# Kernel tuning notes

Measured on AMD Instinct MI355X. Metric: run time of the kernel, lower is better.

## Reference

```python
import jax, jax.numpy as jnp
import numpy as np

D = 1024
H = 8
K = 6
TEMP = 0.1
LN_EPS = 1e-5


def _ln(x, g, b):
    m = jnp.mean(x, axis=-1, keepdims=True)
    v = jnp.mean((x - m) ** 2, axis=-1, keepdims=True)
    return (x - m) / jnp.sqrt(v + LN_EPS) * g + b


def setup_inputs() -> dict:
    key = jax.random.key(0)
    ks = jax.random.split(key, 8)
    B, T = 8, 4096
    s = 0.02
    inp = {
        'video_features': jax.random.normal(ks[0], (B, T, D), jnp.float32),
        'query_embedding': jax.random.normal(ks[1], (B, D), jnp.float32),
        'mu_w1': jax.random.normal(ks[2], (D, D), jnp.float32) * s,
        'mu_b1': jnp.zeros((D,), jnp.float32),
        'mu_g': jnp.ones((D,), jnp.float32),
        'mu_be': jnp.zeros((D,), jnp.float32),
        'mu_w2': jax.random.normal(ks[3], (D, D), jnp.float32) * s,
        'mu_b2': jnp.zeros((D,), jnp.float32),
        'sg_w1': jax.random.normal(ks[4], (D, D), jnp.float32) * s,
        'sg_b1': jnp.zeros((D,), jnp.float32),
        'sg_g': jnp.ones((D,), jnp.float32),
        'sg_be': jnp.zeros((D,), jnp.float32),
        'sg_w2': jax.random.normal(ks[5], (D, D), jnp.float32) * s,
        'sg_b2': jnp.zeros((D,), jnp.float32),
        'in_w': jax.random.normal(ks[6], (3 * D, D), jnp.float32) * s,
        'in_b': jnp.zeros((3 * D,), jnp.float32),
        'out_w': jax.random.normal(ks[7], (D, D), jnp.float32) * s,
        'out_b': jnp.zeros((D,), jnp.float32),
    }
    return inp


def reference(video_features, query_embedding, mu_w1, mu_b1, mu_g, mu_be, mu_w2, mu_b2,
              sg_w1, sg_b1, sg_g, sg_be, sg_w2, sg_b2, in_w, in_b, out_w, out_b):
    B, T, _ = video_features.shape
    dh = D // H

    # mu / sigma estimators (Linear -> LN -> ReLU -> Linear [-> Softplus])
    mu_q = jax.nn.relu(_ln(query_embedding @ mu_w1.T + mu_b1, mu_g, mu_be)) @ mu_w2.T + mu_b2  # [B,D]
    sigma_q = jax.nn.softplus(
        jax.nn.relu(_ln(query_embedding @ sg_w1.T + sg_b1, sg_g, sg_be)) @ sg_w2.T + sg_b2) + 1e-6

    # Mahalanobis (diagonal) distances [B,T]
    centered = video_features - mu_q[:, None, :]
    dist = jnp.sum(centered ** 2 / sigma_q[:, None, :], axis=-1)

    # distance weights around the (torch lower) median
    med = jnp.sort(dist, axis=1)[:, (T - 1) // 2][:, None]
    dist_w = jnp.exp(-jnp.abs(dist - med) / TEMP)  # [B,T]

    # single-query multihead attention (torch MHA, averaged attn weights)
    wq, wk, wv = in_w[:D], in_w[D:2 * D], in_w[2 * D:]
    bq, bk, bv = in_b[:D], in_b[D:2 * D], in_b[2 * D:]
    q = (mu_q @ wq.T + bq).reshape(B, H, dh)                  # [B,H,dh]
    k = (video_features @ wk.T + bk).reshape(B, T, H, dh)     # [B,T,H,dh]
    scores = jnp.einsum('bhd,bthd->bht', q, k) / jnp.sqrt(jnp.asarray(dh, q.dtype))
    attn = jax.nn.softmax(scores, axis=-1)                    # [B,H,T]
    attn_w = jnp.mean(attn, axis=1)                           # [B,T] head-averaged

    combined = dist_w * attn_w  # [B,T]

    # greedy diverse top-k (farthest-point style), vectorized over batch
    ar = jnp.arange(T)
    idx0 = jnp.argmax(combined, axis=1)                       # [B]
    sel_mask = ar[None, :] == idx0[:, None]
    min_d = jnp.abs(ar[None, :] - idx0[:, None]).astype(combined.dtype)
    picks = [idx0]
    for _ in range(K - 1):
        score = jnp.where(sel_mask, -jnp.inf, min_d * combined)
        nxt = jnp.argmax(score, axis=1)
        picks.append(nxt)
        sel_mask = sel_mask | (ar[None, :] == nxt[:, None])
        min_d = jnp.minimum(min_d, jnp.abs(ar[None, :] - nxt[:, None]).astype(combined.dtype))
    indices = jnp.stack(picks, axis=1)  # [B,K]

    rep = jnp.take_along_axis(video_features, indices[:, :, None], axis=1)  # [B,K,D]

    # NTLBG loss
    rep_dist = jnp.take_along_axis(dist, indices, axis=1)  # [B,K]
    target = jnp.sort(rep_dist, axis=1)[:, (K - 1) // 2][:, None]
    ellipsoid = jnp.mean((rep_dist - target) ** 2)
    centered_rep = rep - mu_q[:, None, :]
    consistency = jnp.mean(jnp.sum(centered_rep ** 2 / sigma_q[:, None, :], axis=-1))
    sim = jnp.einsum('bkd,bjd->bkj', rep, rep)
    tri = jnp.triu(jnp.ones((K, K), rep.dtype), k=1)
    diversity = jnp.mean((sim * tri) ** 2)
    loss = ellipsoid + 0.1 * consistency + 0.05 * diversity

    return rep, indices, combined, dist, mu_q, sigma_q, loss
```

## Files before the change

### kernel.cpp

```cpp
#include <hip/hip_runtime.h>
#include <math.h>

#define BD   8
#define TT   4096
#define DD   1024
#define HH   8
#define KK   6
#define OFF_REP   0
#define OFF_IDX   49152
#define OFF_COMB  49200
#define OFF_DIST  81968
#define OFF_MU    114736
#define OFF_SG    122928
#define OFF_LOSS  131120
#define WS_X1     0
#define WS_H      16384
#define WS_Q      32768
#define WS_P      40960
#define WS_C      106496
#define WS_ISIG   106560
#define WS_SCORES 114752

#define INV_SQRT_DH 0.08838834764831845f

__device__ __forceinline__ float softplus_f(float x) {
  return fmaxf(x, 0.0f) + log1pf(expf(-fabsf(x)));
}

__device__ __forceinline__ void gemv_rows_core(const float* __restrict__ in,
                                               const float* __restrict__ W,
                                               int row, float (*s_in)[DD], float acc[8]) {
  int tid = threadIdx.x;
  const float4* in4 = (const float4*)in;
  float4* s4 = (float4*)&s_in[0][0];
  for (int i = tid; i < 2048; i += 256) s4[i] = in4[i];
  __syncthreads();
  int lane = tid & 63;
  const float4* wr4 = (const float4*)(W + (size_t)row * DD);
#pragma unroll
  for (int b = 0; b < 8; ++b) acc[b] = 0.0f;
#pragma unroll
  for (int i = 0; i < 4; ++i) {
    int d4 = i * 64 + lane;
    float4 w4 = wr4[d4];
#pragma unroll
    for (int b = 0; b < 8; ++b) {
      float4 q4 = ((const float4*)&s_in[b][0])[d4];
      acc[b] += w4.x * q4.x + w4.y * q4.y + w4.z * q4.z + w4.w * q4.w;
    }
  }
#pragma unroll
  for (int off = 32; off; off >>= 1)
#pragma unroll
    for (int b = 0; b < 8; ++b) acc[b] += __shfl_xor(acc[b], off, 64);
}

__global__ __launch_bounds__(256) void k_gemv_pre(const float* __restrict__ qe,
    const float* __restrict__ W0, const float* __restrict__ W1,
    const float* __restrict__ b0, const float* __restrict__ b1, float* __restrict__ x1) {
  __shared__ float s_in[8][DD];
  int path = blockIdx.x >> 8;
  int row = (blockIdx.x & 255) * 4 + (threadIdx.x >> 6);
  const float* W = path ? W1 : W0;
  const float* bb = path ? b1 : b0;
  float acc[8];
  gemv_rows_core(qe, W, row, s_in, acc);
  if ((threadIdx.x & 63) == 0) {
    float bv = bb[row];
#pragma unroll
    for (int b = 0; b < 8; ++b) x1[path * 8192 + b * DD + row] = acc[b] + bv;
  }
}

__global__ __launch_bounds__(256) void k_ln(const float* __restrict__ x1,
    const float* __restrict__ g0, const float* __restrict__ be0,
    const float* __restrict__ g1, const float* __restrict__ be1, float* __restrict__ h) {
  int path = blockIdx.x >> 3, b = blockIdx.x & 7;
  const float* x = x1 + path * 8192 + b * DD;
  const float* g = path ? g1 : g0;
  const float* be = path ? be1 : be0;
  __shared__ float sx[DD];
  __shared__ float red[256];
  int tid = threadIdx.x;
  float ps = 0.0f;
  for (int i = tid; i < DD; i += 256) { float v = x[i]; sx[i] = v; ps += v; }
  red[tid] = ps; __syncthreads();
  for (int off = 128; off; off >>= 1) { if (tid < off) red[tid] += red[tid + off]; __syncthreads(); }
  float mean = red[0] * (1.0f / 1024.0f);
  __syncthreads();
  float pv = 0.0f;
  for (int i = tid; i < DD; i += 256) { float d = sx[i] - mean; pv += d * d; }
  red[tid] = pv; __syncthreads();
  for (int off = 128; off; off >>= 1) { if (tid < off) red[tid] += red[tid + off]; __syncthreads(); }
  float var = red[0] * (1.0f / 1024.0f);
  float inv = 1.0f / sqrtf(var + 1e-5f);
  for (int i = tid; i < DD; i += 256) {
    float v = (sx[i] - mean) * inv * g[i] + be[i];
    h[path * 8192 + b * DD + i] = v > 0.0f ? v : 0.0f;
  }
}

__global__ __launch_bounds__(256) void k_gemv_mid(const float* __restrict__ h,
    const float* __restrict__ W0, const float* __restrict__ W1,
    const float* __restrict__ b0, const float* __restrict__ b1,
    float* __restrict__ mu_out, float* __restrict__ sg_out, float* __restrict__ isig) {
  __shared__ float s_in[8][DD];
  int path = blockIdx.x >> 8;
  int row = (blockIdx.x & 255) * 4 + (threadIdx.x >> 6);
  const float* W = path ? W1 : W0;
  const float* bb = path ? b1 : b0;
  float acc[8];
  gemv_rows_core(h + path * 8192, W, row, s_in, acc);
  if ((threadIdx.x & 63) == 0) {
    float bv = bb[row];
#pragma unroll
    for (int b = 0; b < 8; ++b) {
      float v = acc[b] + bv;
      if (path == 0) {
        mu_out[b * DD + row] = v;
      } else {
        float sp = softplus_f(v) + 1e-6f;
        sg_out[b * DD + row] = sp;
        isig[b * DD + row] = 1.0f / sp;
      }
    }
  }
}

__global__ __launch_bounds__(256) void k_gemv_q(const float* __restrict__ mu_q,
    const float* __restrict__ in_w, const float* __restrict__ in_b, float* __restrict__ q) {
  __shared__ float s_in[8][DD];
  int row = blockIdx.x * 4 + (threadIdx.x >> 6);
  float acc[8];
  gemv_rows_core(mu_q, in_w, row, s_in, acc);
  if ((threadIdx.x & 63) == 0) {
    float bv = in_b[row];
#pragma unroll
    for (int b = 0; b < 8; ++b) q[b * DD + row] = acc[b] + bv;
  }
}

__global__ __launch_bounds__(256) void k_p(const float* __restrict__ q,
    const float* __restrict__ in_w, const float* __restrict__ in_b,
    float* __restrict__ p, float* __restrict__ c) {
  int hh = blockIdx.x >> 2;
  int j0 = (blockIdx.x & 3) * 256;
  __shared__ float qh[8][128];
  for (int i = threadIdx.x; i < 1024; i += 256) {
    int b = i >> 7, r = i & 127;
    qh[b][r] = q[b * DD + hh * 128 + r];
  }
  __syncthreads();
  const float* wbase = in_w + (size_t)(DD + hh * 128) * DD + j0 + threadIdx.x;
  float acc[8];
#pragma unroll
  for (int b = 0; b < 8; ++b) acc[b] = 0.0f;
  for (int r = 0; r < 128; ++r) {
    float w = wbase[(size_t)r * DD];
#pragma unroll
    for (int b = 0; b < 8; ++b) acc[b] += qh[b][r] * w;
  }
#pragma unroll
  for (int b = 0; b < 8; ++b) p[(b * HH + hh) * DD + j0 + threadIdx.x] = acc[b] * INV_SQRT_DH;
  if ((blockIdx.x & 3) == 0 && threadIdx.x < 8) {
    int b = threadIdx.x;
    float cc = 0.0f;
    for (int r = 0; r < 128; ++r) cc += qh[b][r] * in_b[DD + hh * 128 + r];
    c[b * HH + hh] = cc * INV_SQRT_DH;
  }
}

__global__ __launch_bounds__(256, 4) void k_main(const float* __restrict__ video,
    const float* __restrict__ mu_q, const float* __restrict__ isig,
    const float* __restrict__ p, const float* __restrict__ c,
    float* __restrict__ dist_out, float* __restrict__ scores, float* __restrict__ loss_out) {
  __shared__ float s_mu[DD];
  __shared__ float s_is[DD];
  __shared__ float s_p[HH][DD];
  int b = blockIdx.x >> 8;
  int chunk = blockIdx.x & 255;
  int tid = threadIdx.x;
  int wave = tid >> 6, lane = tid & 63;
  if (blockIdx.x == 0 && tid == 0) loss_out[0] = 0.0f;
  float4* s_mu4 = (float4*)s_mu;
  float4* s_is4 = (float4*)s_is;
  float4* s_p4 = (float4*)&s_p[0][0];
  s_mu4[tid] = ((const float4*)(mu_q + b * DD))[tid];
  s_is4[tid] = ((const float4*)(isig + b * DD))[tid];
  const float4* pg4 = (const float4*)(p + b * HH * DD);
  for (int i = tid; i < 2048; i += 256) s_p4[i] = pg4[i];
  __syncthreads();

  int t0 = chunk * 16 + wave * 4;
  const float4* v4 = (const float4*)(video + ((size_t)(b * TT + t0)) * DD);
  double dacc[4] = {0.0, 0.0, 0.0, 0.0};
  float sacc[4][8];
#pragma unroll
  for (int t = 0; t < 4; ++t)
#pragma unroll
    for (int hh = 0; hh < 8; ++hh) sacc[t][hh] = 0.0f;

#pragma unroll 2
  for (int i = 0; i < 4; ++i) {
    int d4 = i * 64 + lane;
    float4 vv0 = v4[0 * 256 + d4];
    float4 vv1 = v4[1 * 256 + d4];
    float4 vv2 = v4[2 * 256 + d4];
    float4 vv3 = v4[3 * 256 + d4];
    {
      float4 mu4 = s_mu4[d4];
      float4 is4 = s_is4[d4];
      float dx, dy, dz, dw, e;
      dx = vv0.x - mu4.x; dy = vv0.y - mu4.y; dz = vv0.z - mu4.z; dw = vv0.w - mu4.w;
      e = dx * dx * is4.x + dy * dy * is4.y + dz * dz * is4.z + dw * dw * is4.w;
      dacc[0] += (double)e;
      dx = vv1.x - mu4.x; dy = vv1.y - mu4.y; dz = vv1.z - mu4.z; dw = vv1.w - mu4.w;
      e = dx * dx * is4.x + dy * dy * is4.y + dz * dz * is4.z + dw * dw * is4.w;
      dacc[1] += (double)e;
      dx = vv2.x - mu4.x; dy = vv2.y - mu4.y; dz = vv2.z - mu4.z; dw = vv2.w - mu4.w;
      e = dx * dx * is4.x + dy * dy * is4.y + dz * dz * is4.z + dw * dw * is4.w;
      dacc[2] += (double)e;
      dx = vv3.x - mu4.x; dy = vv3.y - mu4.y; dz = vv3.z - mu4.z; dw = vv3.w - mu4.w;
      e = dx * dx * is4.x + dy * dy * is4.y + dz * dz * is4.z + dw * dw * is4.w;
      dacc[3] += (double)e;
    }
#pragma unroll
    for (int hh = 0; hh < 8; ++hh) {
      float4 pp = ((const float4*)&s_p[hh][0])[d4];
      sacc[0][hh] += pp.x * vv0.x + pp.y * vv0.y + pp.z * vv0.z + pp.w * vv0.w;
      sacc[1][hh] += pp.x * vv1.x + pp.y * vv1.y + pp.z * vv1.z + pp.w * vv1.w;
      sacc[2][hh] += pp.x * vv2.x + pp.y * vv2.y + pp.z * vv2.z + pp.w * vv2.w;
      sacc[3][hh] += pp.x * vv3.x + pp.y * vv3.y + pp.z * vv3.z + pp.w * vv3.w;
    }
  }
#pragma unroll
  for (int off = 32; off; off >>= 1) {
#pragma unroll
    for (int t = 0; t < 4; ++t) {
      dacc[t] += __shfl_xor(dacc[t], off, 64);
#pragma unroll
      for (int hh = 0; hh < 8; ++hh) sacc[t][hh] += __shfl_xor(sacc[t][hh], off, 64);
    }
  }
  if (lane < 4) {
    int t = lane;
    int tt = t0 + t;
    dist_out[b * TT + tt] = (float)dacc[t];
#pragma unroll
    for (int hh = 0; hh < 8; ++hh)
      scores[(size_t)(b * HH + hh) * TT + tt] = sacc[t][hh] + c[b * HH + hh];
  }
}

__global__ __launch_bounds__(256) void k_epilogue(const float* __restrict__ scores,
    const float* __restrict__ dist, const float* __restrict__ video,
    float* __restrict__ comb_out, float* __restrict__ idx_out,
    float* __restrict__ rep, float* __restrict__ loss_out) {
  int b = blockIdx.x;
  int tid = threadIdx.x;
  int wave = tid >> 6, lane = tid & 63;
  __shared__ float s_aw[TT];
  __shared__ float s_comb[TT];
  __shared__ float s_mind[TT];
  __shared__ float s_dist[TT];
  __shared__ float s_hm[HH], s_hs[HH];
  __shared__ unsigned hist[256];
  __shared__ unsigned wsum[4];
  __shared__ unsigned s_sel;
  __shared__ int s_kk;
  __shared__ float wv[4];
  __shared__ int wi[4];
  __shared__ int s_pick;
  __shared__ float wdiv[4];

  {
    int h = tid >> 5, lt = tid & 31;
    const float* srow = scores + ((size_t)(b * HH + h)) * TT;
    float m = -INFINITY;
    for (int i = lt; i < TT; i += 32) m = fmaxf(m, srow[i]);
#pragma unroll
    for (int off = 16; off; off >>= 1) m = fmaxf(m, __shfl_xor(m, off, 64));
    float s = 0.0f;
    for (int i = lt; i < TT; i += 32) s += expf(srow[i] - m);
#pragma unroll
    for (int off = 16; off; off >>= 1) s += __shfl_xor(s, off, 64);
    if (lt == 0) { s_hm[h] = m; s_hs[h] = 1.0f / s; }
  }
  __syncthreads();
  for (int i = tid; i < TT; i += 256) {
    float aw = 0.0f;
#pragma unroll
    for (int h = 0; h < HH; ++h)
      aw += expf(scores[((size_t)(b * HH + h)) * TT + i] - s_hm[h]) * s_hs[h];
    s_aw[i] = aw * 0.125f;
    s_dist[i] = dist[b * TT + i];
  }
  __syncthreads();

  unsigned prefix = 0;
  int kk = (TT - 1) / 2;
  for (int pass = 0; pass < 4; ++pass) {
    int shift = 24 - 8 * pass;
    hist[tid] = 0;
    __syncthreads();
    for (int i = tid; i < TT; i += 256) {
      unsigned key = __float_as_uint(s_dist[i]);
      bool ok = (pass == 0) || ((key >> (shift + 8)) == prefix);
      if (ok) atomicAdd(&hist[(key >> shift) & 255], 1u);
    }
    __syncthreads();
    unsigned h = hist[tid];
    unsigned inc = h;
#pragma unroll
    for (int off = 1; off < 64; off <<= 1) {
      unsigned v = __shfl_up(inc, off, 64);
      if (lane >= off) inc += v;
    }
    if (lane == 63) wsum[wave] = inc;
    __syncthreads();
    unsigned base = 0;
    for (int w = 0; w < wave; ++w) base += wsum[w];
    unsigned excl = base + inc - h;
    if ((int)excl <= kk && kk < (int)(excl + h)) { s_sel = (prefix << 8) | (unsigned)tid; s_kk = kk - (int)excl; }
    __syncthreads();
    prefix = s_sel;
    kk = s_kk;
    __syncthreads();
  }
  float med = __uint_as_float(prefix);

  for (int i = tid; i < TT; i += 256) {
    float cv = expf(-fabsf(s_dist[i] - med) / 0.1f) * s_aw[i];
    s_comb[i] = cv;
    comb_out[b * TT + i] = cv;
  }
  __syncthreads();

  int picks[KK];
  for (int k = 0; k < KK; ++k) {
    float best = -INFINITY; int bi = 1 << 30;
    for (int i = tid; i < TT; i += 256) {
      float cv = s_comb[i];
      float sc = (k == 0) ? cv : ((cv < 0.0f) ? -INFINITY : s_mind[i] * cv);
      if (sc > best) { best = sc; bi = i; }
    }
#pragma unroll
    for (int off = 32; off; off >>= 1) {
      float ov = __shfl_xor(best, off, 64);
      int oi = __shfl_xor(bi, off, 64);
      if (ov > best || (ov == best && oi < bi)) { best = ov; bi = oi; }
    }
    if (lane == 0) { wv[wave] = best; wi[wave] = bi; }
    __syncthreads();
    if (tid == 0) {
      float bb2 = wv[0]; int ii = wi[0];
#pragma unroll
      for (int w = 1; w < 4; ++w)
        if (wv[w] > bb2 || (wv[w] == bb2 && wi[w] < ii)) { bb2 = wv[w]; ii = wi[w]; }
      s_pick = ii;
      s_comb[ii] = -1.0f;
    }
    __syncthreads();
    int pick = s_pick;
    picks[k] = pick;
    for (int i = tid; i < TT; i += 256) {
      float dnew = fabsf((float)(i - pick));
      s_mind[i] = (k == 0) ? dnew : fminf(s_mind[i], dnew);
    }
  }
  if (tid < KK) idx_out[b * KK + tid] = (float)picks[tid];

  __shared__ float repb[KK * DD];
  float4* repb4 = (float4*)repb;
  float4* rep4 = (float4*)(rep + (size_t)b * KK * DD);
  for (int e = tid; e < KK * (DD / 4); e += 256) {
    int k = e >> 8, d4 = e & 255;
    const float4* vrow = (const float4*)(video + ((size_t)(b * TT + picks[0])) * DD);
    vrow = (const float4*)(video + ((size_t)(b * TT + picks[e >> 8])) * DD);
    float4 v = vrow[d4];
    rep4[(size_t)k * (DD / 4) + d4] = v;
    repb4[k * (DD / 4) + d4] = v;
  }
  __syncthreads();
  const int pk[15] = {0,0,0,0,0,1,1,1,1,2,2,2,3,3,4};
  const int pj[15] = {1,2,3,4,5,2,3,4,5,3,4,5,4,5,5};
  float divacc = 0.0f;
  for (int pid = wave; pid < 15; pid += 4) {
    int a = pk[pid], j = pj[pid];
    float part = 0.0f;
    for (int d = lane; d < DD; d += 64) part += repb[a * DD + d] * repb[j * DD + d];
#pragma unroll
    for (int off = 32; off; off >>= 1) part += __shfl_xor(part, off, 64);
    if (lane == 0) divacc += part * part;
  }
  if (lane == 0) wdiv[wave] = divacc;
  __syncthreads();
  if (tid == 0) {
    float div = wdiv[0] + wdiv[1] + wdiv[2] + wdiv[3];
    float rd[KK], srt[KK];
#pragma unroll
    for (int k = 0; k < KK; ++k) { rd[k] = s_dist[picks[k]]; srt[k] = rd[k]; }
    for (int a = 1; a < KK; ++a) {
      float key = srt[a]; int b2 = a - 1;
      while (b2 >= 0 && srt[b2] > key) { srt[b2 + 1] = srt[b2]; --b2; }
      srt[b2 + 1] = key;
    }
    float target = srt[(KK - 1) / 2];
    float ell = 0.0f, cons = 0.0f;
#pragma unroll
    for (int k = 0; k < KK; ++k) { float d = rd[k] - target; ell += d * d; cons += rd[k]; }
    float partial = ell * (1.0f / 48.0f) + 0.1f * cons * (1.0f / 48.0f) + 0.05f * div * (1.0f / 288.0f);
    atomicAdd(loss_out, partial);
  }
}

extern "C" void kernel_launch(void* const* d_in, const int* in_sizes, int n_in,
                              void* d_out, int out_size, void* d_ws, size_t ws_size,
                              hipStream_t stream) {
  const float* video = (const float*)d_in[0];
  const float* qe    = (const float*)d_in[1];
  const float* mu_w1 = (const float*)d_in[2];
  const float* mu_b1 = (const float*)d_in[3];
  const float* mu_g  = (const float*)d_in[4];
  const float* mu_be = (const float*)d_in[5];
  const float* mu_w2 = (const float*)d_in[6];
  const float* mu_b2 = (const float*)d_in[7];
  const float* sg_w1 = (const float*)d_in[8];
  const float* sg_b1 = (const float*)d_in[9];
  const float* sg_g  = (const float*)d_in[10];
  const float* sg_be = (const float*)d_in[11];
  const float* sg_w2 = (const float*)d_in[12];
  const float* sg_b2 = (const float*)d_in[13];
  const float* in_w  = (const float*)d_in[14];
  const float* in_b  = (const float*)d_in[15];
  float* out = (float*)d_out;
  float* ws  = (float*)d_ws;

  k_gemv_pre<<<512, 256, 0, stream>>>(qe, mu_w1, sg_w1, mu_b1, sg_b1, ws + WS_X1);
  k_ln<<<16, 256, 0, stream>>>(ws + WS_X1, mu_g, mu_be, sg_g, sg_be, ws + WS_H);
  k_gemv_mid<<<512, 256, 0, stream>>>(ws + WS_H, mu_w2, sg_w2, mu_b2, sg_b2,
                                      out + OFF_MU, out + OFF_SG, ws + WS_ISIG);
  k_gemv_q<<<256, 256, 0, stream>>>(out + OFF_MU, in_w, in_b, ws + WS_Q);
  k_p<<<32, 256, 0, stream>>>(ws + WS_Q, in_w, in_b, ws + WS_P, ws + WS_C);
  k_main<<<2048, 256, 0, stream>>>(video, out + OFF_MU, ws + WS_ISIG, ws + WS_P, ws + WS_C,
                                   out + OFF_DIST, ws + WS_SCORES, out + OFF_LOSS);
  k_epilogue<<<8, 256, 0, stream>>>(ws + WS_SCORES, out + OFF_DIST, video,
                                    out + OFF_COMB, out + OFF_IDX, out + OFF_REP, out + OFF_LOSS);
}
```

Baseline: 380.7 us.

## Widen epilogue to 1024 threads with register-resident per-thread elements

The per-batch epilogue kernel grows from 256 to 1024 threads. Each thread now keeps four timesteps (distance, attention weight, combined score, min-distance) in registers, read with float4 loads, in place of shared-memory arrays. The softmax reductions, radix-select histogram and greedy farthest-point argmax loops are rewritten for the wider block, and the diversity dot products get one wave per pair. The aim is to cut the serial latency of this 8-block, latency-bound tail, at the cost of more per-block synchronisation across 16 waves.

```diff
diff --git a/kernel.cpp b/kernel.cpp
--- a/kernel.cpp
+++ b/kernel.cpp
@@ -252,76 +252,111 @@
   }
 }
 
-__global__ __launch_bounds__(256) void k_epilogue(const float* __restrict__ scores,
+__global__ __launch_bounds__(1024) void k_epilogue(const float* __restrict__ scores,
     const float* __restrict__ dist, const float* __restrict__ video,
     float* __restrict__ comb_out, float* __restrict__ idx_out,
     float* __restrict__ rep, float* __restrict__ loss_out) {
   int b = blockIdx.x;
   int tid = threadIdx.x;
   int wave = tid >> 6, lane = tid & 63;
-  __shared__ float s_aw[TT];
-  __shared__ float s_comb[TT];
-  __shared__ float s_mind[TT];
   __shared__ float s_dist[TT];
   __shared__ float s_hm[HH], s_hs[HH];
+  __shared__ float s_w16[16], s_w16b[16];
   __shared__ unsigned hist[256];
   __shared__ unsigned wsum[4];
   __shared__ unsigned s_sel;
   __shared__ int s_kk;
-  __shared__ float wv[4];
-  __shared__ int wi[4];
+  __shared__ float wv[16];
+  __shared__ int wi[16];
   __shared__ int s_pick;
-  __shared__ float wdiv[4];
+  __shared__ float wdiv[16];
+  __shared__ float repb[KK * DD];
 
   {
-    int h = tid >> 5, lt = tid & 31;
-    const float* srow = scores + ((size_t)(b * HH + h)) * TT;
+    int h = tid >> 7, lt = tid & 127;
+    const float4* srow4 = (const float4*)(scores + ((size_t)(b * HH + h)) * TT);
     float m = -INFINITY;
-    for (int i = lt; i < TT; i += 32) m = fmaxf(m, srow[i]);
-#pragma unroll
-    for (int off = 16; off; off >>= 1) m = fmaxf(m, __shfl_xor(m, off, 64));
+#pragma unroll
+    for (int i = 0; i < 8; ++i) {
+      float4 v = srow4[lt + i * 128];
+      m = fmaxf(m, fmaxf(fmaxf(v.x, v.y), fmaxf(v.z, v.w)));
+    }
+#pragma unroll
+    for (int off = 32; off; off >>= 1) m = fmaxf(m, __shfl_xor(m, off, 64));
+    if (lane == 0) s_w16[wave] = m;
+    __syncthreads();
+    float mh = fmaxf(s_w16[h * 2], s_w16[h * 2 + 1]);
     float s = 0.0f;
-    for (int i = lt; i < TT; i += 32) s += expf(srow[i] - m);
-#pragma unroll
-    for (int off = 16; off; off >>= 1) s += __shfl_xor(s, off, 64);
-    if (lt == 0) { s_hm[h] = m; s_hs[h] = 1.0f / s; }
-  }
-  __syncthreads();
-  for (int i = tid; i < TT; i += 256) {
-    float aw = 0.0f;
-#pragma unroll
-    for (int h = 0; h < HH; ++h)
-      aw += expf(scores[((size_t)(b * HH + h)) * TT + i] - s_hm[h]) * s_hs[h];
-    s_aw[i] = aw * 0.125f;
-    s_dist[i] = dist[b * TT + i];
-  }
+#pragma unroll
+    for (int i = 0; i < 8; ++i) {
+      float4 v = srow4[lt + i * 128];
+      s += expf(v.x - mh) + expf(v.y - mh) + expf(v.z - mh) + expf(v.w - mh);
+    }
+#pragma unroll
+    for (int off = 32; off; off >>= 1) s += __shfl_xor(s, off, 64);
+    if (lane == 0) s_w16b[wave] = s;
+    __syncthreads();
+    if (lt == 0) { s_hm[h] = mh; s_hs[h] = 1.0f / (s_w16b[h * 2] + s_w16b[h * 2 + 1]); }
+    __syncthreads();
+  }
+
+  float4 d4 = ((const float4*)(dist + b * TT))[tid];
+  ((float4*)s_dist)[tid] = d4;
+  float4 aw = make_float4(0.f, 0.f, 0.f, 0.f);
+#pragma unroll
+  for (int h = 0; h < HH; ++h) {
+    float4 sc = ((const float4*)(scores + ((size_t)(b * HH + h)) * TT))[tid];
+    float mh = s_hm[h], is = s_hs[h];
+    aw.x += expf(sc.x - mh) * is;
+    aw.y += expf(sc.y - mh) * is;
+    aw.z += expf(sc.z - mh) * is;
+    aw.w += expf(sc.w - mh) * is;
+  }
+  aw.x *= 0.125f; aw.y *= 0.125f; aw.z *= 0.125f; aw.w *= 0.125f;
+  uint4 keys;
+  keys.x = __float_as_uint(d4.x);
+  keys.y = __float_as_uint(d4.y);
+  keys.z = __float_as_uint(d4.z);
+  keys.w = __float_as_uint(d4.w);
   __syncthreads();
 
   unsigned prefix = 0;
   int kk = (TT - 1) / 2;
   for (int pass = 0; pass < 4; ++pass) {
     int shift = 24 - 8 * pass;
-    hist[tid] = 0;
-    __syncthreads();
-    for (int i = tid; i < TT; i += 256) {
-      unsigned key = __float_as_uint(s_dist[i]);
-      bool ok = (pass == 0) || ((key >> (shift + 8)) == prefix);
-      if (ok) atomicAdd(&hist[(key >> shift) & 255], 1u);
-    }
-    __syncthreads();
-    unsigned h = hist[tid];
-    unsigned inc = h;
-#pragma unroll
-    for (int off = 1; off < 64; off <<= 1) {
-      unsigned v = __shfl_up(inc, off, 64);
-      if (lane >= off) inc += v;
-    }
-    if (lane == 63) wsum[wave] = inc;
-    __syncthreads();
-    unsigned base = 0;
-    for (int w = 0; w < wave; ++w) base += wsum[w];
-    unsigned excl = base + inc - h;
-    if ((int)excl <= kk && kk < (int)(excl + h)) { s_sel = (prefix << 8) | (unsigned)tid; s_kk = kk - (int)excl; }
+    if (tid < 256) hist[tid] = 0;
+    __syncthreads();
+    {
+      unsigned karr[4] = {keys.x, keys.y, keys.z, keys.w};
+#pragma unroll
+      for (int j = 0; j < 4; ++j) {
+        unsigned key = karr[j];
+        bool ok = (pass == 0) || ((key >> (shift + 8)) == prefix);
+        if (ok) atomicAdd(&hist[(key >> shift) & 255], 1u);
+      }
+    }
+    __syncthreads();
+    unsigned hcnt = 0, inc = 0;
+    if (tid < 256) {
+      hcnt = hist[tid];
+      inc = hcnt;
+#pragma unroll
+      for (int off = 1; off < 64; off <<= 1) {
+        unsigned v = __shfl_up(inc, off, 64);
+        if (lane >= off) inc += v;
+      }
+      if (lane == 63) wsum[wave] = inc;
+    }
+    __syncthreads();
+    if (tid < 256) {
+      unsigned base = 0;
+      for (int w = 0; w < wave; ++w) base += wsum[w];
+      unsigned excl = base + inc - hcnt;
+      if ((int)excl <= kk && kk < (int)(excl + hcnt)) {
+        s_sel = (prefix << 8) | (unsigned)tid;
+        s_kk = kk - (int)excl;
+      }
+    }
     __syncthreads();
     prefix = s_sel;
     kk = s_kk;
@@ -329,20 +364,25 @@
   }
   float med = __uint_as_float(prefix);
 
-  for (int i = tid; i < TT; i += 256) {
-    float cv = expf(-fabsf(s_dist[i] - med) / 0.1f) * s_aw[i];
-    s_comb[i] = cv;
-    comb_out[b * TT + i] = cv;
-  }
-  __syncthreads();
-
+  float4 cb;
+  cb.x = expf(-fabsf(d4.x - med) / 0.1f) * aw.x;
+  cb.y = expf(-fabsf(d4.y - med) / 0.1f) * aw.y;
+  cb.z = expf(-fabsf(d4.z - med) / 0.1f) * aw.z;
+  cb.w = expf(-fabsf(d4.w - med) / 0.1f) * aw.w;
+  ((float4*)(comb_out + b * TT))[tid] = cb;
+
+  float4 md = make_float4(0.f, 0.f, 0.f, 0.f);
+  int i0 = tid * 4;
   int picks[KK];
   for (int k = 0; k < KK; ++k) {
+    float carr[4] = {cb.x, cb.y, cb.z, cb.w};
+    float marr[4] = {md.x, md.y, md.z, md.w};
     float best = -INFINITY; int bi = 1 << 30;
-    for (int i = tid; i < TT; i += 256) {
-      float cv = s_comb[i];
-      float sc = (k == 0) ? cv : ((cv < 0.0f) ? -INFINITY : s_mind[i] * cv);
-      if (sc > best) { best = sc; bi = i; }
+#pragma unroll
+    for (int j = 0; j < 4; ++j) {
+      float cv = carr[j];
+      float sc = (k == 0) ? cv : ((cv < 0.0f) ? -INFINITY : marr[j] * cv);
+      if (sc > best) { best = sc; bi = i0 + j; }
     }
 #pragma unroll
     for (int off = 32; off; off >>= 1) {
@@ -355,48 +395,57 @@
     if (tid == 0) {
       float bb2 = wv[0]; int ii = wi[0];
 #pragma unroll
-      for (int w = 1; w < 4; ++w)
+      for (int w = 1; w < 16; ++w)
         if (wv[w] > bb2 || (wv[w] == bb2 && wi[w] < ii)) { bb2 = wv[w]; ii = wi[w]; }
       s_pick = ii;
-      s_comb[ii] = -1.0f;
     }
     __syncthreads();
     int pick = s_pick;
     picks[k] = pick;
-    for (int i = tid; i < TT; i += 256) {
-      float dnew = fabsf((float)(i - pick));
-      s_mind[i] = (k == 0) ? dnew : fminf(s_mind[i], dnew);
-    }
+    if ((pick >> 2) == tid) {
+      int j = pick & 3;
+      if (j == 0) cb.x = -1.0f; else if (j == 1) cb.y = -1.0f;
+      else if (j == 2) cb.z = -1.0f; else cb.w = -1.0f;
+    }
+    float dn0 = fabsf((float)(i0 + 0 - pick));
+    float dn1 = fabsf((float)(i0 + 1 - pick));
+    float dn2 = fabsf((float)(i0 + 2 - pick));
+    float dn3 = fabsf((float)(i0 + 3 - pick));
+    if (k == 0) { md.x = dn0; md.y = dn1; md.z = dn2; md.w = dn3; }
+    else { md.x = fminf(md.x, dn0); md.y = fminf(md.y, dn1);
+           md.z = fminf(md.z, dn2); md.w = fminf(md.w, dn3); }
   }
   if (tid < KK) idx_out[b * KK + tid] = (float)picks[tid];
 
-  __shared__ float repb[KK * DD];
   float4* repb4 = (float4*)repb;
   float4* rep4 = (float4*)(rep + (size_t)b * KK * DD);
-  for (int e = tid; e < KK * (DD / 4); e += 256) {
-    int k = e >> 8, d4 = e & 255;
-    const float4* vrow = (const float4*)(video + ((size_t)(b * TT + picks[0])) * DD);
-    vrow = (const float4*)(video + ((size_t)(b * TT + picks[e >> 8])) * DD);
-    float4 v = vrow[d4];
-    rep4[(size_t)k * (DD / 4) + d4] = v;
-    repb4[k * (DD / 4) + d4] = v;
-  }
-  __syncthreads();
+  for (int e = tid; e < KK * (DD / 4); e += 1024) {
+    int k = e >> 8, dd4 = e & 255;
+    const float4* vrow = (const float4*)(video + ((size_t)(b * TT + picks[k])) * DD);
+    float4 v = vrow[dd4];
+    rep4[(size_t)k * (DD / 4) + dd4] = v;
+    repb4[e] = v;
+  }
+  __syncthreads();
+
   const int pk[15] = {0,0,0,0,0,1,1,1,1,2,2,2,3,3,4};
   const int pj[15] = {1,2,3,4,5,2,3,4,5,3,4,5,4,5,5};
   float divacc = 0.0f;
-  for (int pid = wave; pid < 15; pid += 4) {
-    int a = pk[pid], j = pj[pid];
+  if (wave < 15) {
+    int a = pk[wave], j = pj[wave];
     float part = 0.0f;
     for (int d = lane; d < DD; d += 64) part += repb[a * DD + d] * repb[j * DD + d];
 #pragma unroll
     for (int off = 32; off; off >>= 1) part += __shfl_xor(part, off, 64);
-    if (lane == 0) divacc += part * part;
-  }
-  if (lane == 0) wdiv[wave] = divacc;
-  __syncthreads();
+    if (lane == 0) divacc = part * part;
+  }
+  if (lane == 0) wdiv[wave] = (wave < 15) ? divacc : 0.0f;
+  __syncthreads();
+
   if (tid == 0) {
-    float div = wdiv[0] + wdiv[1] + wdiv[2] + wdiv[3];
+    float div = 0.0f;
+#pragma unroll
+    for (int w = 0; w < 15; ++w) div += wdiv[w];
     float rd[KK], srt[KK];
 #pragma unroll
     for (int k = 0; k < KK; ++k) { rd[k] = s_dist[picks[k]]; srt[k] = rd[k]; }
@@ -444,6 +493,6 @@
   k_p<<<32, 256, 0, stream>>>(ws + WS_Q, in_w, in_b, ws + WS_P, ws + WS_C);
   k_main<<<2048, 256, 0, stream>>>(video, out + OFF_MU, ws + WS_ISIG, ws + WS_P, ws + WS_C,
                                    out + OFF_DIST, ws + WS_SCORES, out + OFF_LOSS);
-  k_epilogue<<<8, 256, 0, stream>>>(ws + WS_SCORES, out + OFF_DIST, video,
-                                    out + OFF_COMB, out + OFF_IDX, out + OFF_REP, out + OFF_LOSS);
-}
+  k_epilogue<<<8, 1024, 0, stream>>>(ws + WS_SCORES, out + OFF_DIST, video,
+                                     out + OFF_COMB, out + OFF_IDX, out + OFF_REP, out + OFF_LOSS);
+}
```

New measurement: 333.6 us, median of 2. 1.14x faster.
